# Performance work log

Hardware: AMD Instinct MI355X
Metric: run time of the kernel (lower is better)

## Reference

```python
import jax, jax.numpy as jnp
import numpy as np

B, S, D = 4, 4096, 256  # batch, seq, input_dim; q_dim = k_dim = v_dim = D
Q_DIM = 256


def setup_inputs() -> dict:
    key = jax.random.key(0)
    k1, k2, k3, k4 = jax.random.split(key, 4)
    scale = 1.0 / np.sqrt(D)
    return {
        "x_q": jax.random.normal(k1, (B, S, D), dtype=jnp.float32),
        "W_Q": jax.random.normal(k2, (Q_DIM, D), dtype=jnp.float32) * scale,
        "W_K": jax.random.normal(k3, (Q_DIM, D), dtype=jnp.float32) * scale,
        "W_V": jax.random.normal(k4, (Q_DIM, D), dtype=jnp.float32) * scale,
    }


def reference(x_q, W_Q, W_K, W_V):
    # x_k = x_v = x_q (self-attention default path)
    # Linear (bias=False): y = x @ W.T with W of shape (out, in)
    Q = jnp.einsum("bsd,qd->bsq", x_q, W_Q)  # (B, S, q_dim)
    K = jnp.einsum("bsd,kd->bsk", x_q, W_K)  # (B, S, k_dim)
    V = jnp.einsum("bsd,vd->bsv", x_q, W_V)  # (B, S, v_dim)
    scores = jnp.einsum("bqe,bke->bqk", Q, K) / jnp.sqrt(jnp.float32(Q_DIM))
    # NOTE: original uses nn.Softmax(dim=1) -> softmax over the QUERY axis
    attn = jax.nn.softmax(scores, axis=1)  # (B, Sq, Sk)
    return jnp.einsum("bqk,bkv->bqv", attn, V)
```

## Files before the change

### kernel.cpp

```cpp
#include <hip/hip_runtime.h>
#include <hip/hip_bf16.h>


#define BATCH 4
#define SEQ 4096
#define DIM 256
#define ROWS (BATCH * SEQ)

typedef __bf16 bf16x8 __attribute__((ext_vector_type(8)));
typedef float f32x4 __attribute__((ext_vector_type(4)));

#define SB() __builtin_amdgcn_sched_barrier(0)

__device__ __forceinline__ unsigned short f2b(float f) {
    union { float f; unsigned u; } v; v.f = f;
    unsigned u = v.u;
    u += 0x7FFFu + ((u >> 16) & 1u);
    return (unsigned short)(u >> 16);
}

__device__ __forceinline__ float b2f(unsigned short h) {
    union { unsigned u; float f; } v; v.u = ((unsigned)h) << 16;
    return v.f;
}

__global__ void cast_v8(const float* __restrict__ in,
                        unsigned short* __restrict__ out, int n8) {
    int i = blockIdx.x * blockDim.x + threadIdx.x;
    if (i >= n8) return;
    const float4 f0 = *(const float4*)(in + (size_t)i * 8);
    const float4 f1 = *(const float4*)(in + (size_t)i * 8 + 4);
    union { unsigned short u[8]; bf16x8 v; } o;
    o.u[0] = f2b(f0.x); o.u[1] = f2b(f0.y); o.u[2] = f2b(f0.z); o.u[3] = f2b(f0.w);
    o.u[4] = f2b(f1.x); o.u[5] = f2b(f1.y); o.u[6] = f2b(f1.z); o.u[7] = f2b(f1.w);
    *(bf16x8*)(out + (size_t)i * 8) = o.v;
}

__global__ void cast_w3(const float* __restrict__ w0, const float* __restrict__ w1,
                        const float* __restrict__ w2, unsigned short* __restrict__ o0,
                        unsigned short* __restrict__ o1, unsigned short* __restrict__ o2) {
    int t = blockIdx.x * blockDim.x + threadIdx.x;
    int arr = t >> 13;
    int i = (t & 8191);
    const float* in = arr == 0 ? w0 : arr == 1 ? w1 : w2;
    unsigned short* out = arr == 0 ? o0 : arr == 1 ? o1 : o2;
    const float4 f0 = *(const float4*)(in + (size_t)i * 8);
    const float4 f1 = *(const float4*)(in + (size_t)i * 8 + 4);
    union { unsigned short u[8]; bf16x8 v; } o;
    o.u[0] = f2b(f0.x); o.u[1] = f2b(f0.y); o.u[2] = f2b(f0.z); o.u[3] = f2b(f0.w);
    o.u[4] = f2b(f1.x); o.u[5] = f2b(f1.y); o.u[6] = f2b(f1.z); o.u[7] = f2b(f1.w);
    *(bf16x8*)(out + (size_t)i * 8) = o.v;
}

__global__ __launch_bounds__(256) void gemm_qkv(const unsigned short* __restrict__ X,
                                                const unsigned short* __restrict__ Wq,
                                                const unsigned short* __restrict__ Wk,
                                                const unsigned short* __restrict__ Wv,
                                                unsigned short* __restrict__ Qo,
                                                unsigned short* __restrict__ Ko,
                                                unsigned short* __restrict__ Vo) {
    const int z = blockIdx.z;
    const unsigned short* Bw = z == 0 ? Wq : z == 1 ? Wk : Wv;
    unsigned short* out = z == 0 ? Qo : z == 1 ? Ko : Vo;
    const int trans = (z == 2);

    const int l = threadIdx.x & 63;
    const int w = threadIdx.x >> 6;
    const int wr = w >> 1, wc = w & 1;
    const int lr = l & 15, lk = l >> 4;
    const int rbase = blockIdx.x * 128 + wr * 64;
    const int cbase = blockIdx.y * 128 + wc * 64;

    f32x4 acc[4][4] = {};
#pragma unroll
    for (int d0 = 0; d0 < 256; d0 += 32) {
        bf16x8 a[4], b[4];
#pragma unroll
        for (int i = 0; i < 4; ++i)
            a[i] = *(const bf16x8*)(X + (size_t)(rbase + i * 16 + lr) * 256 + d0 + lk * 8);
#pragma unroll
        for (int j = 0; j < 4; ++j)
            b[j] = *(const bf16x8*)(Bw + (size_t)(cbase + j * 16 + lr) * 256 + d0 + lk * 8);
#pragma unroll
        for (int i = 0; i < 4; ++i)
#pragma unroll
            for (int j = 0; j < 4; ++j)
                acc[i][j] = __builtin_amdgcn_mfma_f32_16x16x32_bf16(a[i], b[j], acc[i][j], 0, 0, 0);
    }
#pragma unroll
    for (int i = 0; i < 4; ++i)
#pragma unroll
        for (int j = 0; j < 4; ++j)
#pragma unroll
            for (int r = 0; r < 4; ++r) {
                int row = rbase + i * 16 + lk * 4 + r;
                int col = cbase + j * 16 + lr;
                unsigned short v = f2b(acc[i][j][r]);
                if (!trans) out[(size_t)row * DIM + col] = v;
                else        out[(size_t)col * ROWS + row] = v;
            }
}

__global__ __launch_bounds__(256) void sp_kernel(const unsigned short* __restrict__ Qb,
                                                 const unsigned short* __restrict__ Kb,
                                                 unsigned short* __restrict__ P,
                                                 float* __restrict__ lsum) {
    __shared__ unsigned short smem[32768];
    const int t = threadIdx.x;
    const int w = t >> 6, l = t & 63;
    const int wq = w >> 1, wk = w & 1;
    const int lr = l & 15, lk = l >> 4;
    const int b = blockIdx.z;
    const int kb0 = blockIdx.x * 128;
    const int qb0 = blockIdx.y * 128;
    const unsigned short* Q = Qb + (size_t)b * SEQ * 256;
    const unsigned short* K = Kb + (size_t)b * SEQ * 256;
    unsigned short* Pb = P + (size_t)b * SEQ * SEQ;

    const int lrow = l >> 3;
    const int lslot = l & 7;
    const unsigned short* src[8];
#pragma unroll
    for (int i = 0; i < 8; ++i) {
        const int chunk = i * 4 + w;
        if (chunk < 16) {
            const int arow = chunk * 8 + lrow;
            src[i] = Q + (size_t)(qb0 + arow) * 256 + ((lslot ^ (arow & 7)) * 8);
        } else {
            const int krow = (chunk - 16) * 8 + lrow;
            src[i] = K + (size_t)(kb0 + krow) * 256 + ((lslot ^ (krow & 7)) * 8);
        }
    }

#define SPSTAGE(bi) do {                                                      \
        _Pragma("unroll")                                                     \
        for (int i_ = 0; i_ < 8; ++i_) {                                      \
            const int chunk_ = i_ * 4 + w;                                    \
            __builtin_amdgcn_global_load_lds(                                 \
                (const unsigned int*)src[i_],                                 \
                (unsigned int*)&smem[(bi) * 16384 + chunk_ * 512], 16, 0, 0); \
        }                                                                     \
    } while (0)
#define SPADV() do { _Pragma("unroll") for (int x_ = 0; x_ < 8; ++x_) src[x_] += 64; } while (0)

#define SPCOMPUTE(bi) do {                                                    \
        const char* A_ = (const char*)smem + (bi) * 32768;                    \
        const char* B_ = A_ + 16384;                                          \
        _Pragma("unroll")                                                     \
        for (int ks_ = 0; ks_ < 2; ++ks_) {                                   \
            bf16x8 af_[4], bf_[4];                                            \
            const int cb_ = ks_ * 64 + lk * 16;                               \
            _Pragma("unroll")                                                 \
            for (int i_ = 0; i_ < 4; ++i_) {                                  \
                const int row_ = wq * 64 + i_ * 16 + lr;                      \
                af_[i_] = *(const bf16x8*)(A_ + row_ * 128 +                  \
                                           (cb_ ^ ((row_ & 7) << 4)));        \
            }                                                                 \
            _Pragma("unroll")                                                 \
            for (int j_ = 0; j_ < 4; ++j_) {                                  \
                const int row_ = wk * 64 + j_ * 16 + lr;                      \
                bf_[j_] = *(const bf16x8*)(B_ + row_ * 128 +                  \
                                           (cb_ ^ ((row_ & 7) << 4)));        \
            }                                                                 \
            _Pragma("unroll")                                                 \
            for (int i_ = 0; i_ < 4; ++i_)                                    \
                _Pragma("unroll")                                             \
                for (int j_ = 0; j_ < 4; ++j_)                                \
                    acc[i_][j_] = __builtin_amdgcn_mfma_f32_16x16x32_bf16(    \
                        af_[i_], bf_[j_], acc[i_][j_], 0, 0, 0);              \
        }                                                                     \
    } while (0)

    f32x4 acc[4][4] = {};
    SPSTAGE(0);
#pragma unroll 1
    for (int tt = 0; tt < 4; tt += 2) {
        SPADV();
        SPSTAGE(1);
        SB(); asm volatile("s_waitcnt vmcnt(8)" ::: "memory"); SB();
        __builtin_amdgcn_s_barrier(); SB();
        SPCOMPUTE(0);
        SB(); __builtin_amdgcn_s_barrier(); SB();

        if (tt == 0) {
            SPADV();
            SPSTAGE(0);
            SB(); asm volatile("s_waitcnt vmcnt(8)" ::: "memory"); SB();
        } else {
            SB(); asm volatile("s_waitcnt vmcnt(0)" ::: "memory"); SB();
        }
        __builtin_amdgcn_s_barrier(); SB();
        SPCOMPUTE(1);
        SB(); __builtin_amdgcn_s_barrier(); SB();
    }
#undef SPSTAGE
#undef SPADV
#undef SPCOMPUTE

    unsigned short* Pt = smem;
#pragma unroll
    for (int j = 0; j < 4; ++j) {
        float cs = 0.f;
#pragma unroll
        for (int i = 0; i < 4; ++i)
#pragma unroll
            for (int r = 0; r < 4; ++r) {
                float v = __expf(acc[i][j][r] * 0.0625f);
                cs += v;
                Pt[(wq * 64 + i * 16 + lk * 4 + r) * 136 + wk * 64 + j * 16 + lr] = f2b(v);
            }
        cs += __shfl_xor(cs, 16, 64);
        cs += __shfl_xor(cs, 32, 64);
        if (lk == 0)
            atomicAdd(&lsum[(size_t)b * SEQ + kb0 + wk * 64 + j * 16 + lr], cs);
    }
    __syncthreads();
#pragma unroll
    for (int it = 0; it < 8; ++it) {
        int n = it * 256 + t;
        int row = n >> 4;
        int ch = n & 15;
        *(bf16x8*)(Pb + (size_t)(qb0 + row) * SEQ + kb0 + ch * 8) =
            *(const bf16x8*)(&Pt[row * 136 + ch * 8]);
    }
}

__global__ void scale_vt(unsigned short* __restrict__ Vt,
                         const float* __restrict__ lsum, int n8) {
    int i = blockIdx.x * blockDim.x + threadIdx.x;
    if (i >= n8) return;
    int col8 = (i & (ROWS / 8 - 1)) * 8;
    union { unsigned short u[8]; bf16x8 v; } d;
    d.v = *(const bf16x8*)(Vt + (size_t)i * 8);
#pragma unroll
    for (int j = 0; j < 8; ++j)
        d.u[j] = f2b(b2f(d.u[j]) / lsum[col8 + j]);
    *(bf16x8*)(Vt + (size_t)i * 8) = d.v;
}

__global__ __launch_bounds__(256) void pv_gemm(const unsigned short* __restrict__ P,
                                               const unsigned short* __restrict__ Vt,
                                               float* __restrict__ out) {
    __shared__ unsigned short lds[2][12288];
    const int t = threadIdx.x;
    const int w = t >> 6, l = t & 63;
    const int wq = w >> 1, wv = w & 1;
    const int lr = l & 15, lk = l >> 4;
    const int row_blk = blockIdx.x * 64;
    const int b = row_blk >> 12;
    const int vbase = blockIdx.y * 128;
    const size_t bS = (size_t)b * SEQ;

    const int lrow = l >> 3;
    const int lslot = l & 7;
    const unsigned short* src[6];
#pragma unroll
    for (int i = 0; i < 6; ++i) {
        const int chunk = i * 4 + w;
        if (chunk < 8) {
            const int arow = chunk * 8 + lrow;
            src[i] = P + (size_t)(row_blk + arow) * SEQ + ((lslot ^ (arow & 7)) * 8);
        } else {
            const int vrow = (chunk - 8) * 8 + lrow;
            src[i] = Vt + (size_t)(vbase + vrow) * ROWS + bS + ((lslot ^ (vrow & 7)) * 8);
        }
    }

#define STAGE(bi) do {                                                        \
        _Pragma("unroll")                                                     \
        for (int i_ = 0; i_ < 6; ++i_) {                                      \
            const int chunk_ = i_ * 4 + w;                                    \
            __builtin_amdgcn_global_load_lds(                                 \
                (const unsigned int*)src[i_],                                 \
                (unsigned int*)&lds[bi][chunk_ * 512], 16, 0, 0);             \
        }                                                                     \
    } while (0)

#define ADV() do { _Pragma("unroll") for (int i_ = 0; i_ < 6; ++i_) src[i_] += 64; } while (0)

#define COMPUTE(bi) do {                                                      \
        const char* A_ = (const char*)&lds[bi][0];                            \
        const char* B_ = (const char*)&lds[bi][4096];                         \
        _Pragma("unroll")                                                     \
        for (int ks_ = 0; ks_ < 2; ++ks_) {                                   \
            bf16x8 af_[2], bf_[4];                                            \
            const int cb_ = ks_ * 64 + lk * 16;                               \
            _Pragma("unroll")                                                 \
            for (int i_ = 0; i_ < 2; ++i_) {                                  \
                const int row_ = wq * 32 + i_ * 16 + lr;                      \
                af_[i_] = *(const bf16x8*)(A_ + row_ * 128 +                  \
                                           (cb_ ^ ((row_ & 7) << 4)));        \
            }                                                                 \
            _Pragma("unroll")                                                 \
            for (int j_ = 0; j_ < 4; ++j_) {                                  \
                const int row_ = wv * 64 + j_ * 16 + lr;                      \
                bf_[j_] = *(const bf16x8*)(B_ + row_ * 128 +                  \
                                           (cb_ ^ ((row_ & 7) << 4)));        \
            }                                                                 \
            _Pragma("unroll")                                                 \
            for (int i_ = 0; i_ < 2; ++i_)                                    \
                _Pragma("unroll")                                             \
                for (int j_ = 0; j_ < 4; ++j_)                                \
                    acc[i_][j_] = __builtin_amdgcn_mfma_f32_16x16x32_bf16(    \
                        af_[i_], bf_[j_], acc[i_][j_], 0, 0, 0);              \
        }                                                                     \
    } while (0)

    f32x4 acc[2][4] = {};
    STAGE(0);
#pragma unroll 1
    for (int tt = 0; tt < 64; tt += 2) {
        if (tt < 63) ADV();
        STAGE(1);
        SB(); asm volatile("s_waitcnt vmcnt(6)" ::: "memory"); SB();
        __builtin_amdgcn_s_barrier(); SB();
        COMPUTE(0);
        SB(); __builtin_amdgcn_s_barrier(); SB();

        if (tt + 1 < 63) ADV();
        STAGE(0);
        SB(); asm volatile("s_waitcnt vmcnt(6)" ::: "memory"); SB();
        __builtin_amdgcn_s_barrier(); SB();
        COMPUTE(1);
        SB(); __builtin_amdgcn_s_barrier(); SB();
    }
#undef STAGE
#undef ADV
#undef COMPUTE

#pragma unroll
    for (int i = 0; i < 2; ++i)
#pragma unroll
        for (int j = 0; j < 4; ++j)
#pragma unroll
            for (int r = 0; r < 4; ++r) {
                const int row = row_blk + wq * 32 + i * 16 + lk * 4 + r;
                const int col = vbase + wv * 64 + j * 16 + lr;
                out[(size_t)row * 256 + col] = acc[i][j][r];
            }
}

__global__ __launch_bounds__(256) void colsumexp(const unsigned short* __restrict__ Qb,
                                                 const unsigned short* __restrict__ Kb,
                                                 float* __restrict__ lsum) {
    const int l = threadIdx.x & 63;
    const int w = threadIdx.x >> 6;
    const int wr = w >> 1, wc = w & 1;
    const int lr = l & 15, lk = l >> 4;
    const int b = blockIdx.z;
    const int cbase = blockIdx.x * 128 + wc * 64;
    const unsigned short* Q = Qb + (size_t)b * SEQ * 256;
    const unsigned short* K = Kb + (size_t)b * SEQ * 256;

    float csum[4] = {0.f, 0.f, 0.f, 0.f};
    for (int qi = 0; qi < 16; ++qi) {
        const int rbase = blockIdx.y * 2048 + qi * 128 + wr * 64;
        f32x4 acc[4][4] = {};
#pragma unroll
        for (int d0 = 0; d0 < 256; d0 += 32) {
            bf16x8 a[4], bb[4];
#pragma unroll
            for (int i = 0; i < 4; ++i)
                a[i] = *(const bf16x8*)(Q + (size_t)(rbase + i * 16 + lr) * 256 + d0 + lk * 8);
#pragma unroll
            for (int j = 0; j < 4; ++j)
                bb[j] = *(const bf16x8*)(K + (size_t)(cbase + j * 16 + lr) * 256 + d0 + lk * 8);
#pragma unroll
            for (int i = 0; i < 4; ++i)
#pragma unroll
                for (int j = 0; j < 4; ++j)
                    acc[i][j] = __builtin_amdgcn_mfma_f32_16x16x32_bf16(a[i], bb[j], acc[i][j], 0, 0, 0);
        }
#pragma unroll
        for (int j = 0; j < 4; ++j) {
            float s = 0.f;
#pragma unroll
            for (int i = 0; i < 4; ++i)
#pragma unroll
                for (int r = 0; r < 4; ++r)
                    s += __expf(acc[i][j][r] * 0.0625f);
            csum[j] += s;
        }
    }
#pragma unroll
    for (int j = 0; j < 4; ++j) {
        float s = csum[j];
        s += __shfl_xor(s, 16, 64);
        s += __shfl_xor(s, 32, 64);
        if (lk == 0)
            atomicAdd(&lsum[(size_t)b * SEQ + cbase + j * 16 + lr], s);
    }
}

__global__ __launch_bounds__(256) void pv_kernel(const unsigned short* __restrict__ Qb,
                                                 const unsigned short* __restrict__ Kb,
                                                 const unsigned short* __restrict__ Vt,
                                                 float* __restrict__ out) {
    __shared__ unsigned short Pl[128][72];
    const int l = threadIdx.x & 63;
    const int w = threadIdx.x >> 6;
    const int wr = w >> 1, wc = w & 1;
    const int lr = l & 15, lk = l >> 4;
    const int b = blockIdx.z;
    const int qbase = blockIdx.x * 128;
    const int vbase = blockIdx.y * 128;
    const unsigned short* Q = Qb + (size_t)b * SEQ * 256;
    const unsigned short* K = Kb + (size_t)b * SEQ * 256;
    const unsigned short* V = Vt + (size_t)b * SEQ;

    f32x4 oacc[4][4] = {};
    for (int k0 = 0; k0 < SEQ; k0 += 64) {
        f32x4 sacc[4][2] = {};
#pragma unroll
        for (int d0 = 0; d0 < 256; d0 += 32) {
            bf16x8 a[4], bb[2];
#pragma unroll
            for (int i = 0; i < 4; ++i)
                a[i] = *(const bf16x8*)(Q + (size_t)(qbase + wr * 64 + i * 16 + lr) * 256 + d0 + lk * 8);
#pragma unroll
            for (int j = 0; j < 2; ++j)
                bb[j] = *(const bf16x8*)(K + (size_t)(k0 + wc * 32 + j * 16 + lr) * 256 + d0 + lk * 8);
#pragma unroll
            for (int i = 0; i < 4; ++i)
#pragma unroll
                for (int j = 0; j < 2; ++j)
                    sacc[i][j] = __builtin_amdgcn_mfma_f32_16x16x32_bf16(a[i], bb[j], sacc[i][j], 0, 0, 0);
        }
#pragma unroll
        for (int i = 0; i < 4; ++i)
#pragma unroll
            for (int j = 0; j < 2; ++j)
#pragma unroll
                for (int r = 0; r < 4; ++r)
                    Pl[wr * 64 + i * 16 + lk * 4 + r][wc * 32 + j * 16 + lr] =
                        f2b(__expf(sacc[i][j][r] * 0.0625f));
        __syncthreads();
#pragma unroll
        for (int ks = 0; ks < 2; ++ks) {
            bf16x8 a[4], bb[4];
#pragma unroll
            for (int i = 0; i < 4; ++i)
                a[i] = *(const bf16x8*)(&Pl[wr * 64 + i * 16 + lr][ks * 32 + lk * 8]);
#pragma unroll
            for (int j = 0; j < 4; ++j)
                bb[j] = *(const bf16x8*)(V + (size_t)(vbase + wc * 64 + j * 16 + lr) * ROWS + k0 + ks * 32 + lk * 8);
#pragma unroll
            for (int i = 0; i < 4; ++i)
#pragma unroll
                for (int j = 0; j < 4; ++j)
                    oacc[i][j] = __builtin_amdgcn_mfma_f32_16x16x32_bf16(a[i], bb[j], oacc[i][j], 0, 0, 0);
        }
        __syncthreads();
    }
    float* O = out + (size_t)b * SEQ * 256;
#pragma unroll
    for (int i = 0; i < 4; ++i)
#pragma unroll
        for (int j = 0; j < 4; ++j)
#pragma unroll
            for (int r = 0; r < 4; ++r) {
                int row = qbase + wr * 64 + i * 16 + lk * 4 + r;
                int col = vbase + wc * 64 + j * 16 + lr;
                O[(size_t)row * 256 + col] = oacc[i][j][r];
            }
}

extern "C" void kernel_launch(void* const* d_in, const int* in_sizes, int n_in,
                              void* d_out, int out_size, void* d_ws, size_t ws_size,
                              hipStream_t stream) {
    const float* x  = (const float*)d_in[0];
    const float* wq = (const float*)d_in[1];
    const float* wk = (const float*)d_in[2];
    const float* wv = (const float*)d_in[3];
    float* out = (float*)d_out;

    char* ws = (char*)d_ws;
    unsigned short* Xb  = (unsigned short*)(ws + 0);
    unsigned short* Qb  = (unsigned short*)(ws + 8388608);
    unsigned short* Kb  = (unsigned short*)(ws + 16777216);
    unsigned short* Vt  = (unsigned short*)(ws + 25165824);
    unsigned short* Wqb = (unsigned short*)(ws + 33554432);
    unsigned short* Wkb = (unsigned short*)(ws + 33685504);
    unsigned short* Wvb = (unsigned short*)(ws + 33816576);
    float*          lsum = (float*)(ws + 33947648);
    unsigned short* Pbuf = (unsigned short*)(ws + 34013184);
    const size_t need_A = 34013184 + (size_t)BATCH * SEQ * SEQ * 2;

    const int n_x = ROWS * DIM;

    cast_v8<<<(n_x / 8 + 255) / 256, 256, 0, stream>>>(x, Xb, n_x / 8);
    cast_w3<<<(3 * 8192 + 255) / 256, 256, 0, stream>>>(wq, wk, wv, Wqb, Wkb, Wvb);

    dim3 gg(ROWS / 128, DIM / 128, 3);
    gemm_qkv<<<gg, 256, 0, stream>>>(Xb, Wqb, Wkb, Wvb, Qb, Kb, Vt);

    hipMemsetAsync(lsum, 0, (size_t)BATCH * SEQ * sizeof(float), stream);

    if (ws_size >= need_A) {
        dim3 gs(SEQ / 128, SEQ / 128, BATCH);
        sp_kernel<<<gs, 256, 0, stream>>>(Qb, Kb, Pbuf, lsum);
        scale_vt<<<(n_x / 8 + 255) / 256, 256, 0, stream>>>(Vt, lsum, n_x / 8);
        dim3 gp(ROWS / 64, DIM / 128);
        pv_gemm<<<gp, 256, 0, stream>>>(Pbuf, Vt, out);
    } else {
        dim3 gs(SEQ / 128, 2, BATCH);
        colsumexp<<<gs, 256, 0, stream>>>(Qb, Kb, lsum);
        scale_vt<<<(n_x / 8 + 255) / 256, 256, 0, stream>>>(Vt, lsum, n_x / 8);
        dim3 gp(SEQ / 128, DIM / 128, BATCH);
        pv_kernel<<<gp, 256, 0, stream>>>(Qb, Kb, Vt, out);
    }
}
```

Baseline: 163.2 us.

## Stage QKV GEMM tiles through swizzled LDS with double-buffered async loads

The QKV projection GEMM now loads X and W tiles into a double-buffered, XOR-swizzled shared-memory buffer with global_load_lds, replacing per-wave direct global fragment loads. The next K-slice is prefetched while MFMAs run on the current one, coordinated with explicit vmcnt waits and barriers. This shares tile data across the four waves instead of each wave loading its own overlapping fragments. It adds 64KB of LDS per block, which may lower occupancy, and relies on hand-tuned waitcnt counts. The projection is only a small part of the total attention time.

```diff
diff --git a/kernel.cpp b/kernel.cpp
--- a/kernel.cpp
+++ b/kernel.cpp
@@ -59,34 +59,101 @@
                                                 unsigned short* __restrict__ Qo,
                                                 unsigned short* __restrict__ Ko,
                                                 unsigned short* __restrict__ Vo) {
+    __shared__ unsigned short smem[32768];
     const int z = blockIdx.z;
-    const unsigned short* Bw = z == 0 ? Wq : z == 1 ? Wk : Wv;
-    unsigned short* out = z == 0 ? Qo : z == 1 ? Ko : Vo;
+    const unsigned short* Wz = z == 0 ? Wq : z == 1 ? Wk : Wv;
+    unsigned short* outp = z == 0 ? Qo : z == 1 ? Ko : Vo;
     const int trans = (z == 2);
 
-    const int l = threadIdx.x & 63;
-    const int w = threadIdx.x >> 6;
+    const int t = threadIdx.x;
+    const int w = t >> 6, l = t & 63;
     const int wr = w >> 1, wc = w & 1;
     const int lr = l & 15, lk = l >> 4;
-    const int rbase = blockIdx.x * 128 + wr * 64;
-    const int cbase = blockIdx.y * 128 + wc * 64;
+    const int rb0 = blockIdx.x * 128;
+    const int cb0 = blockIdx.y * 128;
+    const int rbase = rb0 + wr * 64;
+    const int cbase = cb0 + wc * 64;
+
+    const int lrow = l >> 3;
+    const int lslot = l & 7;
+    const unsigned short* src[8];
+#pragma unroll
+    for (int i = 0; i < 8; ++i) {
+        const int chunk = i * 4 + w;
+        if (chunk < 16) {
+            const int xr = chunk * 8 + lrow;
+            src[i] = X + (size_t)(rb0 + xr) * 256 + ((lslot ^ (xr & 7)) * 8);
+        } else {
+            const int wrr = (chunk - 16) * 8 + lrow;
+            src[i] = Wz + (size_t)(cb0 + wrr) * 256 + ((lslot ^ (wrr & 7)) * 8);
+        }
+    }
+
+#define GSTAGE(bi) do {                                                       \
+        _Pragma("unroll")                                                     \
+        for (int i_ = 0; i_ < 8; ++i_) {                                      \
+            const int chunk_ = i_ * 4 + w;                                    \
+            __builtin_amdgcn_global_load_lds(                                 \
+                (const unsigned int*)src[i_],                                 \
+                (unsigned int*)&smem[(bi) * 16384 + chunk_ * 512], 16, 0, 0); \
+        }                                                                     \
+    } while (0)
+#define GADV() do { _Pragma("unroll") for (int x_ = 0; x_ < 8; ++x_) src[x_] += 64; } while (0)
+
+#define GCOMPUTE(bi) do {                                                     \
+        const char* A_ = (const char*)smem + (bi) * 32768;                    \
+        const char* B_ = A_ + 16384;                                          \
+        _Pragma("unroll")                                                     \
+        for (int ks_ = 0; ks_ < 2; ++ks_) {                                   \
+            bf16x8 af_[4], bf_[4];                                            \
+            const int cb_ = ks_ * 64 + lk * 16;                               \
+            _Pragma("unroll")                                                 \
+            for (int i_ = 0; i_ < 4; ++i_) {                                  \
+                const int row_ = wr * 64 + i_ * 16 + lr;                      \
+                af_[i_] = *(const bf16x8*)(A_ + row_ * 128 +                  \
+                                           (cb_ ^ ((row_ & 7) << 4)));        \
+            }                                                                 \
+            _Pragma("unroll")                                                 \
+            for (int j_ = 0; j_ < 4; ++j_) {                                  \
+                const int row_ = wc * 64 + j_ * 16 + lr;                      \
+                bf_[j_] = *(const bf16x8*)(B_ + row_ * 128 +                  \
+                                           (cb_ ^ ((row_ & 7) << 4)));        \
+            }                                                                 \
+            _Pragma("unroll")                                                 \
+            for (int i_ = 0; i_ < 4; ++i_)                                    \
+                _Pragma("unroll")                                             \
+                for (int j_ = 0; j_ < 4; ++j_)                                \
+                    acc[i_][j_] = __builtin_amdgcn_mfma_f32_16x16x32_bf16(    \
+                        af_[i_], bf_[j_], acc[i_][j_], 0, 0, 0);              \
+        }                                                                     \
+    } while (0)
 
     f32x4 acc[4][4] = {};
-#pragma unroll
-    for (int d0 = 0; d0 < 256; d0 += 32) {
-        bf16x8 a[4], b[4];
-#pragma unroll
-        for (int i = 0; i < 4; ++i)
-            a[i] = *(const bf16x8*)(X + (size_t)(rbase + i * 16 + lr) * 256 + d0 + lk * 8);
-#pragma unroll
-        for (int j = 0; j < 4; ++j)
-            b[j] = *(const bf16x8*)(Bw + (size_t)(cbase + j * 16 + lr) * 256 + d0 + lk * 8);
-#pragma unroll
-        for (int i = 0; i < 4; ++i)
-#pragma unroll
-            for (int j = 0; j < 4; ++j)
-                acc[i][j] = __builtin_amdgcn_mfma_f32_16x16x32_bf16(a[i], b[j], acc[i][j], 0, 0, 0);
-    }
+    GSTAGE(0);
+#pragma unroll 1
+    for (int tt = 0; tt < 4; tt += 2) {
+        GADV();
+        GSTAGE(1);
+        SB(); asm volatile("s_waitcnt vmcnt(8)" ::: "memory"); SB();
+        __builtin_amdgcn_s_barrier(); SB();
+        GCOMPUTE(0);
+        SB(); __builtin_amdgcn_s_barrier(); SB();
+
+        if (tt == 0) {
+            GADV();
+            GSTAGE(0);
+            SB(); asm volatile("s_waitcnt vmcnt(8)" ::: "memory"); SB();
+        } else {
+            SB(); asm volatile("s_waitcnt vmcnt(0)" ::: "memory"); SB();
+        }
+        __builtin_amdgcn_s_barrier(); SB();
+        GCOMPUTE(1);
+        SB(); __builtin_amdgcn_s_barrier(); SB();
+    }
+#undef GSTAGE
+#undef GADV
+#undef GCOMPUTE
+
 #pragma unroll
     for (int i = 0; i < 4; ++i)
 #pragma unroll
@@ -96,8 +163,8 @@
                 int row = rbase + i * 16 + lk * 4 + r;
                 int col = cbase + j * 16 + lr;
                 unsigned short v = f2b(acc[i][j][r]);
-                if (!trans) out[(size_t)row * DIM + col] = v;
-                else        out[(size_t)col * ROWS + row] = v;
+                if (!trans) outp[(size_t)row * DIM + col] = v;
+                else        outp[(size_t)col * ROWS + row] = v;
             }
 }
 
```

Result: faster. 153.6 us (-5.9%).
